# Kernel tuning notes

Measured on AMD Instinct MI355X. Metric: run time of the kernel, lower is better.

Reference implementation:

```python
import jax, jax.numpy as jnp
import numpy as np

N_NODES = 100000
D_FEAT = 128
N_EDGES = 1600000


def setup_inputs() -> dict:
    key = jax.random.key(0)
    k1, k2, k3 = jax.random.split(key, 3)
    node_tensor = jax.random.normal(k1, (N_NODES, D_FEAT), dtype=jnp.float32)
    edge_src = jax.random.randint(k2, (N_EDGES,), 0, N_NODES, dtype=jnp.int64)
    edge_dst = jax.random.randint(k3, (N_EDGES,), 0, N_NODES, dtype=jnp.int64)
    return {"node_tensor": node_tensor, "edge_src": edge_src, "edge_dst": edge_dst}


def reference(node_tensor, edge_src, edge_dst):
    # Depth-1 neighbourhood traversal: for each node, neighbourhood = {self} U {src of incoming edges}.
    # Mean reducer over the neighbourhood features, then concat onto node features (dim=1),
    # mirroring NodeGraphNeighbourhood.forward with include_self=True.
    n = node_tensor.shape[0]
    gathered = node_tensor[edge_src]                      # [E, D] irregular gather
    neigh_sum = jax.ops.segment_sum(gathered, edge_dst, num_segments=n)   # [N, D]
    deg = jax.ops.segment_sum(jnp.ones(edge_dst.shape[0], dtype=node_tensor.dtype),
                              edge_dst, num_segments=n)   # [N]
    reduced = (neigh_sum + node_tensor) / (deg + 1.0)[:, None]            # mean incl. self
    return jnp.concatenate((node_tensor, reduced), axis=1)               # [N, 2D]
```

## Files before the change

kernel.cpp:

```cpp
#include <hip/hip_runtime.h>

#define DFEAT 128
#define NBK_SHIFT 6
#define BNODES 64
#define CAP 1536
#define CHUNK 16384
#define NBMAX 1600

typedef float v2f __attribute__((ext_vector_type(2)));


struct SmemScatter {
    int lcnt[NBMAX];
    int part[512];
    unsigned spair[CHUNK];
};

__device__ __forceinline__ void convert_item(const float4* __restrict__ node4,
                                             uint2* __restrict__ nf,
                                             float4* __restrict__ out4, int t) {
    float4 a = node4[2 * t];
    float4 b = node4[2 * t + 1];
    unsigned lo = 0, hi = 0;
    lo = __builtin_amdgcn_cvt_pk_fp8_f32(a.x, a.y, lo, false);
    lo = __builtin_amdgcn_cvt_pk_fp8_f32(a.z, a.w, lo, true);
    hi = __builtin_amdgcn_cvt_pk_fp8_f32(b.x, b.y, hi, false);
    hi = __builtin_amdgcn_cvt_pk_fp8_f32(b.z, b.w, hi, true);
    nf[t] = make_uint2(lo, hi);
    int n = t >> 4;
    int j = t & 15;
    size_t orow = (size_t)n * 64;
    out4[orow + 2 * j] = a;
    out4[orow + 2 * j + 1] = b;
}

__device__ void scatter_chunk(SmemScatter& sm, const int4* __restrict__ src4,
                              const int4* __restrict__ dst4,
                              unsigned* __restrict__ pairbuf, int* __restrict__ glofs,
                              int chunk, int n_quads, int n_edges, int nb) {
    int tid = threadIdx.x;
    for (int i = tid; i < nb; i += 512) sm.lcnt[i] = 0;
    __syncthreads();

    int e0 = chunk * CHUNK;
    int e1 = min(e0 + CHUNK, n_edges);
    int q0 = e0 >> 2;
    int q1 = min(q0 + CHUNK / 4, n_quads);
    int ccnt = e1 - e0;

    for (int q = q0 + tid; q < q1; q += 512) {
        int4 d = dst4[q];
        int base = q * 4;
        if (base + 3 < n_edges) {
            atomicAdd(&sm.lcnt[d.x >> NBK_SHIFT], 1);
            atomicAdd(&sm.lcnt[d.y >> NBK_SHIFT], 1);
            atomicAdd(&sm.lcnt[d.z >> NBK_SHIFT], 1);
            atomicAdd(&sm.lcnt[d.w >> NBK_SHIFT], 1);
        } else {
            const int* dd = (const int*)&d;
            for (int k = 0; k < 4 && base + k < n_edges; ++k)
                atomicAdd(&sm.lcnt[dd[k] >> NBK_SHIFT], 1);
        }
    }
    __syncthreads();

    int* lrow = glofs + (size_t)chunk * (nb + 1);
    {
        int t4 = tid * 4;
        int s = 0;
#pragma unroll
        for (int k = 0; k < 4; ++k) {
            int idx = t4 + k;
            if (idx < nb) s += sm.lcnt[idx];
        }
        sm.part[tid] = s;
        __syncthreads();
        for (int d = 1; d < 512; d <<= 1) {
            int v = sm.part[tid];
            int a = (tid >= d) ? sm.part[tid - d] : 0;
            __syncthreads();
            sm.part[tid] = v + a;
            __syncthreads();
        }
        int run = sm.part[tid] - s;
#pragma unroll
        for (int k = 0; k < 4; ++k) {
            int idx = t4 + k;
            if (idx < nb) {
                int c = sm.lcnt[idx];
                lrow[idx] = run;
                sm.lcnt[idx] = run;
                run += c;
            }
        }
        if (tid == 0) lrow[nb] = ccnt;
    }
    __syncthreads();

    for (int q = q0 + tid; q < q1; q += 512) {
        int4 s = src4[q];
        int4 d = dst4[q];
        int base = q * 4;
        const int* ss = (const int*)&s;
        const int* dd = (const int*)&d;
        int kmax = (base + 3 < n_edges) ? 4 : (n_edges - base);
        for (int k = 0; k < kmax; ++k) {
            int dv = dd[k];
            int b = dv >> NBK_SHIFT;
            int pos = atomicAdd(&sm.lcnt[b], 1);
            sm.spair[pos] = ((unsigned)(dv & (BNODES - 1)) << 17) | (unsigned)ss[k];
        }
    }
    __syncthreads();

    unsigned* pout = pairbuf + (size_t)chunk * CHUNK;
    for (int i = tid; i < ccnt; i += 512) pout[i] = sm.spair[i];
}

__global__ void __launch_bounds__(512)
ngn_prep_kernel(const float4* __restrict__ node4,
                const int4* __restrict__ src4, const int4* __restrict__ dst4,
                uint2* __restrict__ nf, unsigned* __restrict__ pairbuf,
                int* __restrict__ glofs, float4* __restrict__ out4,
                int n_edges, int nb, int nchunks, int total_cv) {
    __shared__ SmemScatter sm;
    int bid = blockIdx.x;
    int n_quads = (n_edges + 3) >> 2;
    if (bid < nchunks) {
        scatter_chunk(sm, src4, dst4, pairbuf, glofs, bid, n_quads, n_edges, nb);
    } else {
        int t = (bid - nchunks) * 512 + threadIdx.x;
        if (t < total_cv) convert_item(node4, nf, out4, t);
    }
}

__device__ __forceinline__ void acc8_fp8(uint2 w, float& a0, float& a1, float& a2, float& a3,
                                         float& a4, float& a5, float& a6, float& a7) {
    v2f f0 = __builtin_amdgcn_cvt_pk_f32_fp8(w.x, false);
    v2f f1 = __builtin_amdgcn_cvt_pk_f32_fp8(w.x, true);
    v2f f2 = __builtin_amdgcn_cvt_pk_f32_fp8(w.y, false);
    v2f f3 = __builtin_amdgcn_cvt_pk_f32_fp8(w.y, true);
    a0 += f0.x; a1 += f0.y; a2 += f1.x; a3 += f1.y;
    a4 += f2.x; a5 += f2.y; a6 += f3.x; a7 += f3.y;
}

__global__ void __launch_bounds__(256)
ngn_passB_kernel(const float4* __restrict__ node4,
                 const uint2* __restrict__ nf2,
                 const unsigned* __restrict__ pairbuf,
                 const int* __restrict__ glofs,
                 float4* __restrict__ out4, int n_nodes, int nchunks, int nb) {
    __shared__ int lhist[BNODES];
    __shared__ int loff[BNODES];
    __shared__ int lcur[BNODES];
    __shared__ int part[256];
    __shared__ unsigned stage[CAP];
    __shared__ unsigned srt[CAP];

    int bid = blockIdx.x;
    int xcd = bid & 7;
    int idx = bid >> 3;
    int qq = nb >> 3, rr = nb & 7;
    int b = (xcd < rr ? xcd * (qq + 1) : rr * (qq + 1) + (xcd - rr) * qq) + idx;

    int node0 = b << NBK_SHIFT;
    int nnodes = min(BNODES, n_nodes - node0);
    int tid = threadIdx.x;
    int wave = tid >> 6, lane = tid & 63;
    int q = lane >> 4;
    int fl = lane & 15;

    int tot = 0;
    for (int c = tid; c < nchunks; c += 256) {
        const int* lrow = glofs + (size_t)c * (nb + 1);
        tot += lrow[b + 1] - lrow[b];
    }
    part[tid] = tot;
    __syncthreads();
    for (int d = 1; d < 256; d <<= 1) {
        int v = part[tid];
        int a = (tid >= d) ? part[tid - d] : 0;
        __syncthreads();
        part[tid] = v + a;
        __syncthreads();
    }
    int base = part[tid] - tot;
    int cnt = min(part[255], CAP);
    int pos = base;
    for (int c = tid; c < nchunks; c += 256) {
        const int* lrow = glofs + (size_t)c * (nb + 1);
        int s0 = lrow[b], s1 = lrow[b + 1];
        const unsigned* pin = pairbuf + (size_t)c * CHUNK;
        for (int j = s0; j < s1; ++j) {
            if (pos < CAP) stage[pos] = pin[j];
            ++pos;
        }
    }
    __syncthreads();

    if (tid < BNODES) lhist[tid] = 0;
    __syncthreads();
    for (int i = tid; i < cnt; i += 256) atomicAdd(&lhist[stage[i] >> 17], 1);
    __syncthreads();
    if (wave == 0) {
        int v = lhist[lane];
        int p = v;
        for (int d = 1; d < 64; d <<= 1) {
            int t2 = __shfl_up(p, d);
            if (lane >= d) p += t2;
        }
        loff[lane] = p - v;
        lcur[lane] = p - v;
    }
    __syncthreads();
    for (int i = tid; i < cnt; i += 256) {
        unsigned p = stage[i];
        int pp = atomicAdd(&lcur[p >> 17], 1);
        srt[pp] = p & 0x1FFFFu;
    }
    __syncthreads();

    for (int l = wave; l < nnodes; l += 4) {
        int o0 = loff[l];
        int deg = lhist[l];
        int n = node0 + l;
        float a0 = 0.f, a1 = 0.f, a2 = 0.f, a3 = 0.f;
        float a4 = 0.f, a5 = 0.f, a6 = 0.f, a7 = 0.f;
        int i = 0;
        for (; i + 16 <= deg; i += 16) {
            int s0 = srt[o0 + i + q];
            int s1 = srt[o0 + i + 4 + q];
            int s2 = srt[o0 + i + 8 + q];
            int s3 = srt[o0 + i + 12 + q];
            uint2 w0 = nf2[(size_t)s0 * 16 + fl];
            uint2 w1 = nf2[(size_t)s1 * 16 + fl];
            uint2 w2 = nf2[(size_t)s2 * 16 + fl];
            uint2 w3 = nf2[(size_t)s3 * 16 + fl];
            acc8_fp8(w0, a0, a1, a2, a3, a4, a5, a6, a7);
            acc8_fp8(w1, a0, a1, a2, a3, a4, a5, a6, a7);
            acc8_fp8(w2, a0, a1, a2, a3, a4, a5, a6, a7);
            acc8_fp8(w3, a0, a1, a2, a3, a4, a5, a6, a7);
        }
        for (; i + 4 <= deg; i += 4) {
            int s0 = srt[o0 + i + q];
            uint2 w0 = nf2[(size_t)s0 * 16 + fl];
            acc8_fp8(w0, a0, a1, a2, a3, a4, a5, a6, a7);
        }
        int rem = deg - i;
        if (q < rem) {
            int s0 = srt[o0 + i + q];
            uint2 w0 = nf2[(size_t)s0 * 16 + fl];
            acc8_fp8(w0, a0, a1, a2, a3, a4, a5, a6, a7);
        }
        a0 += __shfl_xor(a0, 16); a1 += __shfl_xor(a1, 16);
        a2 += __shfl_xor(a2, 16); a3 += __shfl_xor(a3, 16);
        a4 += __shfl_xor(a4, 16); a5 += __shfl_xor(a5, 16);
        a6 += __shfl_xor(a6, 16); a7 += __shfl_xor(a7, 16);
        a0 += __shfl_xor(a0, 32); a1 += __shfl_xor(a1, 32);
        a2 += __shfl_xor(a2, 32); a3 += __shfl_xor(a3, 32);
        a4 += __shfl_xor(a4, 32); a5 += __shfl_xor(a5, 32);
        a6 += __shfl_xor(a6, 32); a7 += __shfl_xor(a7, 32);
        if (q == 0) {
            float4 s0 = node4[(size_t)n * 32 + 2 * fl];
            float4 s1 = node4[(size_t)n * 32 + 2 * fl + 1];
            float inv = 1.0f / (float)(deg + 1);
            float4 r0, r1;
            r0.x = (a0 + s0.x) * inv; r0.y = (a1 + s0.y) * inv;
            r0.z = (a2 + s0.z) * inv; r0.w = (a3 + s0.w) * inv;
            r1.x = (a4 + s1.x) * inv; r1.y = (a5 + s1.y) * inv;
            r1.z = (a6 + s1.z) * inv; r1.w = (a7 + s1.w) * inv;
            out4[(size_t)n * 64 + 32 + 2 * fl] = r0;
            out4[(size_t)n * 64 + 32 + 2 * fl + 1] = r1;
        }
    }
}

extern "C" void kernel_launch(void* const* d_in, const int* in_sizes, int n_in,
                              void* d_out, int out_size, void* d_ws, size_t ws_size,
                              hipStream_t stream) {
    const float4* node4 = (const float4*)d_in[0];
    const int4* src4 = (const int4*)d_in[1];
    const int4* dst4 = (const int4*)d_in[2];
    float4* out4 = (float4*)d_out;

    int n_nodes = in_sizes[0] / DFEAT;
    int n_edges = in_sizes[1];
    int nb = (n_nodes + BNODES - 1) >> NBK_SHIFT;
    int nchunks = (n_edges + CHUNK - 1) / CHUNK;
    int total_cv = n_nodes * (DFEAT / 8);

    uint2* nf = (uint2*)d_ws;
    unsigned* pairbuf = (unsigned*)(nf + (size_t)n_nodes * (DFEAT / 8));
    int* glofs = (int*)(pairbuf + (size_t)nchunks * CHUNK);

    int cv_blocks = (total_cv + 511) / 512;
    ngn_prep_kernel<<<nchunks + cv_blocks, 512, 0, stream>>>(
        node4, src4, dst4, nf, pairbuf, glofs, out4, n_edges, nb, nchunks, total_cv);

    ngn_passB_kernel<<<nb, 256, 0, stream>>>(node4, nf, pairbuf, glofs, out4,
                                             n_nodes, nchunks, nb);
}
```

Measured before the change: 89.48 us.

## Transpose segment-offset table and widen fp8 gathers to 16-byte loads

The per-chunk bucket offset table is now stored bucket-major, so each pass-B block reads its two offset rows contiguously instead of striding across chunk rows. The gather loop switches from 8-byte to 16-byte fp8 row loads. Each lane now covers 16 features and a wave processes 8 neighbours per step instead of 4. This cuts the number of load instructions and makes the offset reads coalesced. In exchange it needs an extra shuffle-reduction stage and 16 accumulators per lane, which raises register pressure.

```diff
diff --git a/kernel.cpp b/kernel.cpp
--- a/kernel.cpp
+++ b/kernel.cpp
@@ -36,8 +36,8 @@
 
 __device__ void scatter_chunk(SmemScatter& sm, const int4* __restrict__ src4,
                               const int4* __restrict__ dst4,
-                              unsigned* __restrict__ pairbuf, int* __restrict__ glofs,
-                              int chunk, int n_quads, int n_edges, int nb) {
+                              unsigned* __restrict__ pairbuf, int* __restrict__ gseg,
+                              int chunk, int n_quads, int n_edges, int nb, int nchunks) {
     int tid = threadIdx.x;
     for (int i = tid; i < nb; i += 512) sm.lcnt[i] = 0;
     __syncthreads();
@@ -64,7 +64,6 @@
     }
     __syncthreads();
 
-    int* lrow = glofs + (size_t)chunk * (nb + 1);
     {
         int t4 = tid * 4;
         int s = 0;
@@ -88,12 +87,12 @@
             int idx = t4 + k;
             if (idx < nb) {
                 int c = sm.lcnt[idx];
-                lrow[idx] = run;
+                gseg[(size_t)idx * nchunks + chunk] = run;
                 sm.lcnt[idx] = run;
                 run += c;
             }
         }
-        if (tid == 0) lrow[nb] = ccnt;
+        if (tid == 0) gseg[(size_t)nb * nchunks + chunk] = ccnt;
     }
     __syncthreads();
 
@@ -121,34 +120,37 @@
 ngn_prep_kernel(const float4* __restrict__ node4,
                 const int4* __restrict__ src4, const int4* __restrict__ dst4,
                 uint2* __restrict__ nf, unsigned* __restrict__ pairbuf,
-                int* __restrict__ glofs, float4* __restrict__ out4,
+                int* __restrict__ gseg, float4* __restrict__ out4,
                 int n_edges, int nb, int nchunks, int total_cv) {
     __shared__ SmemScatter sm;
     int bid = blockIdx.x;
     int n_quads = (n_edges + 3) >> 2;
     if (bid < nchunks) {
-        scatter_chunk(sm, src4, dst4, pairbuf, glofs, bid, n_quads, n_edges, nb);
+        scatter_chunk(sm, src4, dst4, pairbuf, gseg, bid, n_quads, n_edges, nb, nchunks);
     } else {
         int t = (bid - nchunks) * 512 + threadIdx.x;
         if (t < total_cv) convert_item(node4, nf, out4, t);
     }
 }
 
-__device__ __forceinline__ void acc8_fp8(uint2 w, float& a0, float& a1, float& a2, float& a3,
-                                         float& a4, float& a5, float& a6, float& a7) {
-    v2f f0 = __builtin_amdgcn_cvt_pk_f32_fp8(w.x, false);
-    v2f f1 = __builtin_amdgcn_cvt_pk_f32_fp8(w.x, true);
-    v2f f2 = __builtin_amdgcn_cvt_pk_f32_fp8(w.y, false);
-    v2f f3 = __builtin_amdgcn_cvt_pk_f32_fp8(w.y, true);
-    a0 += f0.x; a1 += f0.y; a2 += f1.x; a3 += f1.y;
-    a4 += f2.x; a5 += f2.y; a6 += f3.x; a7 += f3.y;
+__device__ __forceinline__ void acc4_fp8(unsigned u, float& a, float& b, float& c, float& d) {
+    v2f f0 = __builtin_amdgcn_cvt_pk_f32_fp8(u, false);
+    v2f f1 = __builtin_amdgcn_cvt_pk_f32_fp8(u, true);
+    a += f0.x; b += f0.y; c += f1.x; d += f1.y;
+}
+
+__device__ __forceinline__ void acc16_fp8(uint4 v, float* a) {
+    acc4_fp8(v.x, a[0], a[1], a[2], a[3]);
+    acc4_fp8(v.y, a[4], a[5], a[6], a[7]);
+    acc4_fp8(v.z, a[8], a[9], a[10], a[11]);
+    acc4_fp8(v.w, a[12], a[13], a[14], a[15]);
 }
 
 __global__ void __launch_bounds__(256)
 ngn_passB_kernel(const float4* __restrict__ node4,
-                 const uint2* __restrict__ nf2,
+                 const uint4* __restrict__ nf4,
                  const unsigned* __restrict__ pairbuf,
-                 const int* __restrict__ glofs,
+                 const int* __restrict__ gseg,
                  float4* __restrict__ out4, int n_nodes, int nchunks, int nb) {
     __shared__ int lhist[BNODES];
     __shared__ int loff[BNODES];
@@ -167,14 +169,14 @@
     int nnodes = min(BNODES, n_nodes - node0);
     int tid = threadIdx.x;
     int wave = tid >> 6, lane = tid & 63;
-    int q = lane >> 4;
-    int fl = lane & 15;
+    int q = lane >> 3;
+    int fl = lane & 7;
+
+    const int* rowb = gseg + (size_t)b * nchunks;
+    const int* rowb1 = gseg + (size_t)(b + 1) * nchunks;
 
     int tot = 0;
-    for (int c = tid; c < nchunks; c += 256) {
-        const int* lrow = glofs + (size_t)c * (nb + 1);
-        tot += lrow[b + 1] - lrow[b];
-    }
+    for (int c = tid; c < nchunks; c += 256) tot += rowb1[c] - rowb[c];
     part[tid] = tot;
     __syncthreads();
     for (int d = 1; d < 256; d <<= 1) {
@@ -188,8 +190,7 @@
     int cnt = min(part[255], CAP);
     int pos = base;
     for (int c = tid; c < nchunks; c += 256) {
-        const int* lrow = glofs + (size_t)c * (nb + 1);
-        int s0 = lrow[b], s1 = lrow[b + 1];
+        int s0 = rowb[c], s1 = rowb1[c];
         const unsigned* pin = pairbuf + (size_t)c * CHUNK;
         for (int j = s0; j < s1; ++j) {
             if (pos < CAP) stage[pos] = pin[j];
@@ -224,53 +225,50 @@
         int o0 = loff[l];
         int deg = lhist[l];
         int n = node0 + l;
-        float a0 = 0.f, a1 = 0.f, a2 = 0.f, a3 = 0.f;
-        float a4 = 0.f, a5 = 0.f, a6 = 0.f, a7 = 0.f;
+        float a[16];
+#pragma unroll
+        for (int k = 0; k < 16; ++k) a[k] = 0.f;
         int i = 0;
         for (; i + 16 <= deg; i += 16) {
             int s0 = srt[o0 + i + q];
-            int s1 = srt[o0 + i + 4 + q];
-            int s2 = srt[o0 + i + 8 + q];
-            int s3 = srt[o0 + i + 12 + q];
-            uint2 w0 = nf2[(size_t)s0 * 16 + fl];
-            uint2 w1 = nf2[(size_t)s1 * 16 + fl];
-            uint2 w2 = nf2[(size_t)s2 * 16 + fl];
-            uint2 w3 = nf2[(size_t)s3 * 16 + fl];
-            acc8_fp8(w0, a0, a1, a2, a3, a4, a5, a6, a7);
-            acc8_fp8(w1, a0, a1, a2, a3, a4, a5, a6, a7);
-            acc8_fp8(w2, a0, a1, a2, a3, a4, a5, a6, a7);
-            acc8_fp8(w3, a0, a1, a2, a3, a4, a5, a6, a7);
-        }
-        for (; i + 4 <= deg; i += 4) {
+            int s1 = srt[o0 + i + 8 + q];
+            uint4 w0 = nf4[(size_t)s0 * 8 + fl];
+            uint4 w1 = nf4[(size_t)s1 * 8 + fl];
+            acc16_fp8(w0, a);
+            acc16_fp8(w1, a);
+        }
+        if (i + 8 <= deg) {
             int s0 = srt[o0 + i + q];
-            uint2 w0 = nf2[(size_t)s0 * 16 + fl];
-            acc8_fp8(w0, a0, a1, a2, a3, a4, a5, a6, a7);
+            uint4 w0 = nf4[(size_t)s0 * 8 + fl];
+            acc16_fp8(w0, a);
+            i += 8;
         }
         int rem = deg - i;
         if (q < rem) {
             int s0 = srt[o0 + i + q];
-            uint2 w0 = nf2[(size_t)s0 * 16 + fl];
-            acc8_fp8(w0, a0, a1, a2, a3, a4, a5, a6, a7);
-        }
-        a0 += __shfl_xor(a0, 16); a1 += __shfl_xor(a1, 16);
-        a2 += __shfl_xor(a2, 16); a3 += __shfl_xor(a3, 16);
-        a4 += __shfl_xor(a4, 16); a5 += __shfl_xor(a5, 16);
-        a6 += __shfl_xor(a6, 16); a7 += __shfl_xor(a7, 16);
-        a0 += __shfl_xor(a0, 32); a1 += __shfl_xor(a1, 32);
-        a2 += __shfl_xor(a2, 32); a3 += __shfl_xor(a3, 32);
-        a4 += __shfl_xor(a4, 32); a5 += __shfl_xor(a5, 32);
-        a6 += __shfl_xor(a6, 32); a7 += __shfl_xor(a7, 32);
+            uint4 w0 = nf4[(size_t)s0 * 8 + fl];
+            acc16_fp8(w0, a);
+        }
+#pragma unroll
+        for (int k = 0; k < 16; ++k) {
+            a[k] += __shfl_xor(a[k], 8);
+            a[k] += __shfl_xor(a[k], 16);
+            a[k] += __shfl_xor(a[k], 32);
+        }
         if (q == 0) {
-            float4 s0 = node4[(size_t)n * 32 + 2 * fl];
-            float4 s1 = node4[(size_t)n * 32 + 2 * fl + 1];
             float inv = 1.0f / (float)(deg + 1);
-            float4 r0, r1;
-            r0.x = (a0 + s0.x) * inv; r0.y = (a1 + s0.y) * inv;
-            r0.z = (a2 + s0.z) * inv; r0.w = (a3 + s0.w) * inv;
-            r1.x = (a4 + s1.x) * inv; r1.y = (a5 + s1.y) * inv;
-            r1.z = (a6 + s1.z) * inv; r1.w = (a7 + s1.w) * inv;
-            out4[(size_t)n * 64 + 32 + 2 * fl] = r0;
-            out4[(size_t)n * 64 + 32 + 2 * fl + 1] = r1;
+            size_t srow = (size_t)n * 32;
+            size_t orow = (size_t)n * 64;
+#pragma unroll
+            for (int c = 0; c < 4; ++c) {
+                float4 s = node4[srow + 4 * fl + c];
+                float4 r;
+                r.x = (a[4 * c + 0] + s.x) * inv;
+                r.y = (a[4 * c + 1] + s.y) * inv;
+                r.z = (a[4 * c + 2] + s.z) * inv;
+                r.w = (a[4 * c + 3] + s.w) * inv;
+                out4[orow + 32 + 4 * fl + c] = r;
+            }
         }
     }
 }
@@ -291,12 +289,12 @@
 
     uint2* nf = (uint2*)d_ws;
     unsigned* pairbuf = (unsigned*)(nf + (size_t)n_nodes * (DFEAT / 8));
-    int* glofs = (int*)(pairbuf + (size_t)nchunks * CHUNK);
+    int* gseg = (int*)(pairbuf + (size_t)nchunks * CHUNK);
 
     int cv_blocks = (total_cv + 511) / 512;
     ngn_prep_kernel<<<nchunks + cv_blocks, 512, 0, stream>>>(
-        node4, src4, dst4, nf, pairbuf, glofs, out4, n_edges, nb, nchunks, total_cv);
-
-    ngn_passB_kernel<<<nb, 256, 0, stream>>>(node4, nf, pairbuf, glofs, out4,
-                                             n_nodes, nchunks, nb);
-}
+        node4, src4, dst4, nf, pairbuf, gseg, out4, n_edges, nb, nchunks, total_cv);
+
+    ngn_passB_kernel<<<nb, 256, 0, stream>>>(node4, (const uint4*)nf, pairbuf, gseg,
+                                             out4, n_nodes, nchunks, nb);
+}
```

Result: slower. 116.1 us (+29.8%).
